# Performance work log

Hardware: AMD Instinct MI355X
Metric: run time of the kernel (lower is better)

The kernel has to match this reference:

```python
import jax, jax.numpy as jnp
import numpy as np

K = 1024          # num_embeddings
D = 128           # embedding_dim
COMMITMENT_COST = 0.25


def setup_inputs() -> dict:
    key = jax.random.key(0)
    k1, k2 = jax.random.split(key)
    inputs = jax.random.normal(k1, (16, D, 4096), dtype=jnp.float32)
    codebook = jax.random.normal(k2, (K, D), dtype=jnp.float32)
    return {"inputs": inputs, "codebook": codebook}


def reference(inputs, codebook):
    # inputs: [B, D, T]; codebook: [K, D]
    B, Dd, T = inputs.shape
    flat = jnp.transpose(inputs, (0, 2, 1)).reshape(-1, Dd)  # [N, D], N = B*T
    N = flat.shape[0]

    d = (jnp.sum(flat * flat, axis=1, keepdims=True)
         + jnp.sum(codebook * codebook, axis=1)
         - 2.0 * flat @ codebook.T)
    idx = jnp.argmin(d, axis=1)  # [N]

    # gather-based quantization (same math as one-hot @ codebook)
    quantized = codebook[idx]                                   # [N, D]
    quantized = quantized.reshape(B, T, Dd).transpose(0, 2, 1)  # [B, D, T]

    # commitment loss (quantized detached; stop_gradient irrelevant in fwd)
    e_latent_loss = jnp.mean((jax.lax.stop_gradient(quantized) - inputs) ** 2)
    loss = COMMITMENT_COST * e_latent_loss

    # straight-through estimator
    quantized_st = inputs + jax.lax.stop_gradient(quantized - inputs)

    # perplexity from code usage histogram (= mean of one-hot encodings)
    counts = jnp.zeros((codebook.shape[0],), dtype=jnp.float32).at[idx].add(1.0)
    avg_probs = counts / N
    perplexity = jnp.exp(-jnp.sum(avg_probs * jnp.log(avg_probs + 1e-10)))

    return loss, quantized_st, perplexity, idx.reshape(B, T)
```

## Files before the change

kernel.cpp:

```cpp
#include <hip/hip_runtime.h>

#define T_FULL 4096
#define D 128
#define K 1024
#define NVEC 65536
#define BDT 8388608
#define BT 128
#define NBLK (NVEC / BT)
#define KT 64
#define NIT (K / KT)
#define PLANE_B (K * D * 2)
#define TILE_B (2 * KT * D * 2)

typedef _Float16 f16x8 __attribute__((ext_vector_type(8)));
typedef float f32x4 __attribute__((ext_vector_type(4)));

#define MFMA(a, b, c) __builtin_amdgcn_mfma_f32_16x16x32_f16((a), (b), (c), 0, 0, 0)

#define GLOAD_LDS(g, l)                                                        \
  __builtin_amdgcn_global_load_lds(                                            \
      (const __attribute__((address_space(1))) unsigned int*)(g),              \
      (__attribute__((address_space(3))) unsigned int*)(l), 16, 0, 0)

__global__ __launch_bounds__(128) void prep_kernel(const float* __restrict__ cb,
    float* __restrict__ ee, _Float16* __restrict__ E1, _Float16* __restrict__ E2,
    unsigned int* __restrict__ counts, unsigned int* __restrict__ done,
    float* __restrict__ loss_acc) {
  int k = blockIdx.x, d = threadIdx.x;
  if (d == 0) {
    counts[k] = 0u;
    if (k == 0) { *done = 0u; *loss_acc = 0.f; }
  }
  float e = cb[k * D + d];
  float v = e * e;
#pragma unroll
  for (int o = 32; o > 0; o >>= 1) v += __shfl_down(v, o, 64);
  __shared__ float tmp[2];
  if ((d & 63) == 0) tmp[d >> 6] = v;
  __syncthreads();
  if (d == 0) ee[k] = tmp[0] + tmp[1];

  float s = 2.0f * e;
  _Float16 h1 = (_Float16)s;
  _Float16 h2 = (_Float16)(s - (float)h1);
  E1[k * D + d] = h1;
  E2[k * D + d] = h2;
}

__global__ __launch_bounds__(256, 2) void vq_main(
    const float* __restrict__ inp, const float* __restrict__ cb,
    const float* __restrict__ ee, const _Float16* __restrict__ Eplanes,
    unsigned int* __restrict__ counts, unsigned int* __restrict__ done,
    float* __restrict__ loss_acc, float* __restrict__ out) {
  __shared__ __align__(16) _Float16 Bs[2 * 2 * KT * D];
  __shared__ float ee_sh[K];
  __shared__ int   midx[BT];
  __shared__ float lred[4];
  __shared__ int   lastf;

  float* out_q   = out + 1;
  float* out_idx = out + 2 + BDT;

  const int tid  = threadIdx.x;
  const int lane = tid & 63;
  const int w    = tid >> 6;
  const int c    = lane & 15;
  const int q    = lane >> 4;
  const int b    = blockIdx.x >> 5;
  const int t0   = (blockIdx.x & 31) * BT;

  unsigned soff[8], slds[8];
#pragma unroll
  for (int i = 0; i < 8; ++i) {
    int flat = tid + i * 256;
    int p    = flat >> 10;
    int s    = flat & 1023;
    int code = s >> 4;
    int dgp  = s & 15;
    int dg   = dgp ^ (code & 15);
    soff[i] = (unsigned)(p * PLANE_B + code * 256 + dg * 16);
    slds[i] = (unsigned)(flat * 16);
  }
  const char* Eb = (const char*)Eplanes;

#pragma unroll
  for (int i = 0; i < 8; ++i)
    GLOAD_LDS(Eb + soff[i], (char*)Bs + slds[i]);

  f16x8 A1[2][4], A2[2][4];
  {
    const float* xin = inp + (size_t)b * D * T_FULL + t0 + w * 32 + c;
#pragma unroll
    for (int n = 0; n < 2; ++n)
#pragma unroll
      for (int dc = 0; dc < 4; ++dc) {
        f16x8 a1, a2;
#pragma unroll
        for (int j = 0; j < 8; ++j) {
          int d = dc * 32 + q * 8 + j;
          float x = xin[(size_t)d * T_FULL + n * 16];
          _Float16 h1 = (_Float16)x;
          _Float16 h2 = (_Float16)(x - (float)h1);
          a1[j] = h1; a2[j] = h2;
        }
        A1[n][dc] = a1; A2[n][dc] = a2;
      }
  }
#pragma unroll
  for (int i = tid; i < K; i += 256) ee_sh[i] = ee[i];
  __syncthreads();

  float bv[2][4];
  int   bi[2][4];
#pragma unroll
  for (int n = 0; n < 2; ++n)
#pragma unroll
    for (int r = 0; r < 4; ++r) { bv[n][r] = 3.4e38f; bi[n][r] = 0; }

  for (int it = 0; it < NIT; ++it) {
    const int kt = it * KT;
    const int bb = it & 1;

    if (it) __syncthreads();

    if (it != NIT - 1) {
      const int ktn = kt + KT;
      const unsigned lbo = (unsigned)((bb ^ 1) * TILE_B);
#pragma unroll
      for (int i = 0; i < 8; ++i)
        GLOAD_LDS(Eb + (size_t)ktn * 256 + soff[i], (char*)Bs + lbo + slds[i]);
    }

    f32x4 acc[2][4];
#pragma unroll
    for (int n = 0; n < 2; ++n)
#pragma unroll
      for (int kf = 0; kf < 4; ++kf) acc[n][kf] = (f32x4){0.f, 0.f, 0.f, 0.f};

    const char* Bp = (const char*)Bs + bb * TILE_B;
#pragma unroll
    for (int dc = 0; dc < 4; ++dc) {
      const int sw = ((dc * 4 + q) ^ c) * 16;
      f16x8 B1[4], B2[4];
#pragma unroll
      for (int kf = 0; kf < 4; ++kf) {
        const int ro = (kf * 16 + c) * 256 + sw;
        B1[kf] = *(const f16x8*)(Bp + ro);
        B2[kf] = *(const f16x8*)(Bp + 16384 + ro);
      }
#pragma unroll
      for (int n = 0; n < 2; ++n)
#pragma unroll
        for (int kf = 0; kf < 4; ++kf) {
          f32x4 a = acc[n][kf];
          a = MFMA(A1[n][dc], B1[kf], a);
          a = MFMA(A1[n][dc], B2[kf], a);
          a = MFMA(A2[n][dc], B1[kf], a);
          acc[n][kf] = a;
        }
    }

#pragma unroll
    for (int kf = 0; kf < 4; ++kf) {
      const int code = kt + kf * 16 + c;
      const float eev = ee_sh[code];
#pragma unroll
      for (int n = 0; n < 2; ++n)
#pragma unroll
        for (int r = 0; r < 4; ++r) {
          float dist = eev - acc[n][kf][r];
          if (dist < bv[n][r]) { bv[n][r] = dist; bi[n][r] = code; }
        }
    }
  }

#pragma unroll
  for (int m = 1; m <= 8; m <<= 1)
#pragma unroll
    for (int n = 0; n < 2; ++n)
#pragma unroll
      for (int r = 0; r < 4; ++r) {
        float ov = __shfl_xor(bv[n][r], m, 64);
        int   oi = __shfl_xor(bi[n][r], m, 64);
        if (ov < bv[n][r] || (ov == bv[n][r] && oi < bi[n][r])) {
          bv[n][r] = ov; bi[n][r] = oi;
        }
      }
  if (c == 0) {
#pragma unroll
    for (int n = 0; n < 2; ++n)
#pragma unroll
      for (int r = 0; r < 4; ++r)
        midx[w * 32 + n * 16 + q * 4 + r] = bi[n][r];
  }
  __syncthreads();

  if (tid < BT) {
    int ki = midx[tid];
    out_idx[(size_t)b * T_FULL + t0 + tid] = (float)ki;
    atomicAdd(&counts[ki], 1u);
  }

  float lsum = 0.f;
  {
    const int t  = tid & 127;
    const int dh = tid >> 7;
    const int kq = midx[t];
    const float* crow = cb + (size_t)kq * D + dh * 64;
    const float* xrow = inp + ((size_t)b * D + dh * 64) * T_FULL + t0 + t;
    float*       qrow = out_q + ((size_t)b * D + dh * 64) * T_FULL + t0 + t;
#pragma unroll
    for (int dd = 0; dd < 64; dd += 4) {
      float4 qv = *(const float4*)(crow + dd);
      float x0 = xrow[(size_t)(dd + 0) * T_FULL];
      float x1 = xrow[(size_t)(dd + 1) * T_FULL];
      float x2 = xrow[(size_t)(dd + 2) * T_FULL];
      float x3 = xrow[(size_t)(dd + 3) * T_FULL];
      float df;
      df = qv.x - x0; lsum = fmaf(df, df, lsum); qrow[(size_t)(dd + 0) * T_FULL] = qv.x;
      df = qv.y - x1; lsum = fmaf(df, df, lsum); qrow[(size_t)(dd + 1) * T_FULL] = qv.y;
      df = qv.z - x2; lsum = fmaf(df, df, lsum); qrow[(size_t)(dd + 2) * T_FULL] = qv.z;
      df = qv.w - x3; lsum = fmaf(df, df, lsum); qrow[(size_t)(dd + 3) * T_FULL] = qv.w;
    }
  }
#pragma unroll
  for (int o = 32; o > 0; o >>= 1) lsum += __shfl_down(lsum, o, 64);
  if (lane == 0) lred[w] = lsum;
  __syncthreads();
  if (tid == 0) {
    atomicAdd(loss_acc, lred[0] + lred[1] + lred[2] + lred[3]);
    __threadfence();
    unsigned ticket = atomicAdd(done, 1u);
    lastf = (ticket == NBLK - 1) ? 1 : 0;
  }
  __syncthreads();

  if (lastf) {
    __threadfence();
    float ent = 0.f;
#pragma unroll
    for (int i = tid; i < K; i += 256) {
      float cnt = (float)atomicAdd(&counts[i], 0u);
      float p = cnt * (1.0f / (float)NVEC);
      ent = fmaf(p, logf(p + 1e-10f), ent);
    }
#pragma unroll
    for (int o = 32; o > 0; o >>= 1) ent += __shfl_down(ent, o, 64);
    if (lane == 0) lred[w] = ent;
    __syncthreads();
    if (tid == 0) {
      float e = lred[0] + lred[1] + lred[2] + lred[3];
      float l = atomicAdd(loss_acc, 0.f);
      out[0]       = 0.25f * (l / (float)BDT);
      out[1 + BDT] = expf(-e);
    }
  }
}

extern "C" void kernel_launch(void* const* d_in, const int* in_sizes, int n_in,
                              void* d_out, int out_size, void* d_ws, size_t ws_size,
                              hipStream_t stream) {
  const float* inp = (const float*)d_in[0];
  const float* cb  = (const float*)d_in[1];
  float* out = (float*)d_out;

  char* ws = (char*)d_ws;
  unsigned int* counts  = (unsigned int*)ws;
  unsigned int* done    = (unsigned int*)(ws + 4096);
  float*        lossacc = (float*)(ws + 4160);
  float*        ee      = (float*)(ws + 8192);
  _Float16*     E1      = (_Float16*)(ws + 12288);
  _Float16*     E2      = (_Float16*)(ws + 12288 + PLANE_B);

  prep_kernel<<<K, 128, 0, stream>>>(cb, ee, E1, E2, counts, done, lossacc);
  vq_main<<<NBLK, 256, 0, stream>>>(inp, cb, ee, E1, counts, done, lossacc, out);
}
```

Baseline: 184.6 us.

## Deepen codebook LDS pipeline to four smaller buffers with manual vmcnt waits

Halves the codebook tile to 32 codes and uses four LDS buffers, prefetching two tiles ahead with explicit s_waitcnt vmcnt counts and raw s_barrier instead of __syncthreads. It also splits each accumulator into a main term and a correction term, breaking the three-MFMA dependency chain, and raises wave priority around the MFMA block. The goal is to hide global-to-LDS latency and improve MFMA issue. The risk is that the manual vmcnt counts are wrong or the barriers do not cover buffer reuse, which could cause races; smaller tiles also add per-iteration overhead.

```diff
diff --git a/kernel.cpp b/kernel.cpp
--- a/kernel.cpp
+++ b/kernel.cpp
@@ -7,10 +7,13 @@
 #define BDT 8388608
 #define BT 128
 #define NBLK (NVEC / BT)
-#define KT 64
+#define KT 32
 #define NIT (K / KT)
+#define NBUF 4
 #define PLANE_B (K * D * 2)
 #define TILE_B (2 * KT * D * 2)
+#define TPLANE (KT * D * 2)
+#define GTILE (KT * D * 2)
 
 typedef _Float16 f16x8 __attribute__((ext_vector_type(8)));
 typedef float f32x4 __attribute__((ext_vector_type(4)));
@@ -21,6 +24,9 @@
   __builtin_amdgcn_global_load_lds(                                            \
       (const __attribute__((address_space(1))) unsigned int*)(g),              \
       (__attribute__((address_space(3))) unsigned int*)(l), 16, 0, 0)
+
+#define SBAR() __builtin_amdgcn_s_barrier()
+#define SFENCE() __builtin_amdgcn_sched_barrier(0)
 
 __global__ __launch_bounds__(128) void prep_kernel(const float* __restrict__ cb,
     float* __restrict__ ee, _Float16* __restrict__ E1, _Float16* __restrict__ E2,
@@ -52,7 +58,7 @@
     const float* __restrict__ ee, const _Float16* __restrict__ Eplanes,
     unsigned int* __restrict__ counts, unsigned int* __restrict__ done,
     float* __restrict__ loss_acc, float* __restrict__ out) {
-  __shared__ __align__(16) _Float16 Bs[2 * 2 * KT * D];
+  __shared__ __align__(16) _Float16 Bs[NBUF * 2 * KT * D];
   __shared__ float ee_sh[K];
   __shared__ int   midx[BT];
   __shared__ float lred[4];
@@ -69,12 +75,12 @@
   const int b    = blockIdx.x >> 5;
   const int t0   = (blockIdx.x & 31) * BT;
 
-  unsigned soff[8], slds[8];
-#pragma unroll
-  for (int i = 0; i < 8; ++i) {
+  unsigned soff[4], slds[4];
+#pragma unroll
+  for (int i = 0; i < 4; ++i) {
     int flat = tid + i * 256;
-    int p    = flat >> 10;
-    int s    = flat & 1023;
+    int p    = flat >> 9;
+    int s    = flat & 511;
     int code = s >> 4;
     int dgp  = s & 15;
     int dg   = dgp ^ (code & 15);
@@ -84,8 +90,10 @@
   const char* Eb = (const char*)Eplanes;
 
 #pragma unroll
-  for (int i = 0; i < 8; ++i)
-    GLOAD_LDS(Eb + soff[i], (char*)Bs + slds[i]);
+  for (int t = 0; t < 2; ++t)
+#pragma unroll
+    for (int i = 0; i < 4; ++i)
+      GLOAD_LDS(Eb + (size_t)t * GTILE + soff[i], (char*)Bs + t * TILE_B + slds[i]);
 
   f16x8 A1[2][4], A2[2][4];
   {
@@ -117,62 +125,77 @@
 #pragma unroll
     for (int r = 0; r < 4; ++r) { bv[n][r] = 3.4e38f; bi[n][r] = 0; }
 
-  for (int it = 0; it < NIT; ++it) {
-    const int kt = it * KT;
-    const int bb = it & 1;
-
-    if (it) __syncthreads();
-
-    if (it != NIT - 1) {
-      const int ktn = kt + KT;
-      const unsigned lbo = (unsigned)((bb ^ 1) * TILE_B);
-#pragma unroll
-      for (int i = 0; i < 8; ++i)
-        GLOAD_LDS(Eb + (size_t)ktn * 256 + soff[i], (char*)Bs + lbo + slds[i]);
+#define COMPUTE_TILE(IT)                                                       \
+  {                                                                            \
+    const int   kt_ = (IT) * KT;                                               \
+    const char* Bp  = (const char*)Bs + ((IT) & (NBUF - 1)) * TILE_B;          \
+    f32x4 accM[2][2], accC[2][2];                                              \
+    _Pragma("unroll")                                                          \
+    for (int n = 0; n < 2; ++n)                                                \
+      _Pragma("unroll")                                                        \
+      for (int kf = 0; kf < 2; ++kf) {                                         \
+        accM[n][kf] = (f32x4){0.f, 0.f, 0.f, 0.f};                             \
+        accC[n][kf] = (f32x4){0.f, 0.f, 0.f, 0.f};                             \
+      }                                                                        \
+    __builtin_amdgcn_s_setprio(1);                                             \
+    _Pragma("unroll")                                                          \
+    for (int dc = 0; dc < 4; ++dc) {                                           \
+      const int sw = ((dc * 4 + q) ^ c) * 16;                  \
+      f16x8 B1[2], B2[2];                                                      \
+      _Pragma("unroll")                                                        \
+      for (int kf = 0; kf < 2; ++kf) {                                         \
+        const int ro = (kf * 16 + c) * 256 + sw;                               \
+        B1[kf] = *(const f16x8*)(Bp + ro);                                     \
+        B2[kf] = *(const f16x8*)(Bp + TPLANE + ro);                            \
+      }                                                                        \
+      _Pragma("unroll")                                                        \
+      for (int n = 0; n < 2; ++n)                                              \
+        _Pragma("unroll")                                                      \
+        for (int kf = 0; kf < 2; ++kf) {                                       \
+          accM[n][kf] = MFMA(A1[n][dc], B1[kf], accM[n][kf]);                  \
+          f32x4 t_ = accC[n][kf];                                              \
+          t_ = MFMA(A1[n][dc], B2[kf], t_);                                    \
+          t_ = MFMA(A2[n][dc], B1[kf], t_);                                    \
+          accC[n][kf] = t_;                                                    \
+        }                                                                      \
+    }                                                                          \
+    __builtin_amdgcn_s_setprio(0);                                             \
+    _Pragma("unroll")                                                          \
+    for (int kf = 0; kf < 2; ++kf) {                                           \
+      const int   code = kt_ + kf * 16 + c;                                    \
+      const float eev  = ee_sh[code];                                          \
+      _Pragma("unroll")                                                        \
+      for (int n = 0; n < 2; ++n)                                              \
+        _Pragma("unroll")                                                      \
+        for (int r = 0; r < 4; ++r) {                                          \
+          float dist = eev - accM[n][kf][r] - accC[n][kf][r];                  \
+          if (dist < bv[n][r]) { bv[n][r] = dist; bi[n][r] = code; }           \
+        }                                                                      \
+    }                                                                          \
+  }
+
+  for (int it = 0; it < NIT - 2; ++it) {
+    {
+      const char* gs = Eb + (size_t)(it + 2) * GTILE;
+      char*       ld = (char*)Bs + ((it + 2) & (NBUF - 1)) * TILE_B;
+#pragma unroll
+      for (int i = 0; i < 4; ++i) GLOAD_LDS(gs + soff[i], ld + slds[i]);
     }
-
-    f32x4 acc[2][4];
-#pragma unroll
-    for (int n = 0; n < 2; ++n)
-#pragma unroll
-      for (int kf = 0; kf < 4; ++kf) acc[n][kf] = (f32x4){0.f, 0.f, 0.f, 0.f};
-
-    const char* Bp = (const char*)Bs + bb * TILE_B;
-#pragma unroll
-    for (int dc = 0; dc < 4; ++dc) {
-      const int sw = ((dc * 4 + q) ^ c) * 16;
-      f16x8 B1[4], B2[4];
-#pragma unroll
-      for (int kf = 0; kf < 4; ++kf) {
-        const int ro = (kf * 16 + c) * 256 + sw;
-        B1[kf] = *(const f16x8*)(Bp + ro);
-        B2[kf] = *(const f16x8*)(Bp + 16384 + ro);
-      }
-#pragma unroll
-      for (int n = 0; n < 2; ++n)
-#pragma unroll
-        for (int kf = 0; kf < 4; ++kf) {
-          f32x4 a = acc[n][kf];
-          a = MFMA(A1[n][dc], B1[kf], a);
-          a = MFMA(A1[n][dc], B2[kf], a);
-          a = MFMA(A2[n][dc], B1[kf], a);
-          acc[n][kf] = a;
-        }
-    }
-
-#pragma unroll
-    for (int kf = 0; kf < 4; ++kf) {
-      const int code = kt + kf * 16 + c;
-      const float eev = ee_sh[code];
-#pragma unroll
-      for (int n = 0; n < 2; ++n)
-#pragma unroll
-        for (int r = 0; r < 4; ++r) {
-          float dist = eev - acc[n][kf][r];
-          if (dist < bv[n][r]) { bv[n][r] = dist; bi[n][r] = code; }
-        }
-    }
-  }
+    SFENCE();
+    asm volatile("s_waitcnt vmcnt(8)" ::: "memory");
+    SBAR();
+    SFENCE();
+    COMPUTE_TILE(it);
+  }
+  asm volatile("s_waitcnt vmcnt(4)" ::: "memory");
+  SBAR();
+  SFENCE();
+  COMPUTE_TILE(NIT - 2);
+  asm volatile("s_waitcnt vmcnt(0)" ::: "memory");
+  SBAR();
+  SFENCE();
+  COMPUTE_TILE(NIT - 1);
+#undef COMPUTE_TILE
 
 #pragma unroll
   for (int m = 1; m <= 8; m <<= 1)
```

Measured after the change: 186.2 us. Within noise of the previous version (+0.8%).

## Halve block and codebook tiles to double occupancy, split MFMA accumulator chains

Applied to the files above, without the earlier changes.

Cuts the per-block vector tile from 128 to 64 and the codebook tile from 64 to 32 codes. Each wave now handles one 16-row fragment, which shrinks the register and LDS footprint so four blocks can run per CU instead of two. The fp16 hi/lo MFMA chain is split into a main accumulator and a correction accumulator, giving two independent dependency chains for more instruction-level parallelism. In exchange, each wave reuses every LDS codebook read across fewer MFMAs, and codebook traffic from L2 doubles because twice as many blocks stream the whole codebook.

```diff
diff --git a/kernel.cpp b/kernel.cpp
--- a/kernel.cpp
+++ b/kernel.cpp
@@ -5,12 +5,14 @@
 #define K 1024
 #define NVEC 65536
 #define BDT 8388608
-#define BT 128
+#define BT 64
 #define NBLK (NVEC / BT)
-#define KT 64
+#define KT 32
 #define NIT (K / KT)
 #define PLANE_B (K * D * 2)
 #define TILE_B (2 * KT * D * 2)
+#define TPLANE (KT * D * 2)
+#define GTILE (KT * D * 2)
 
 typedef _Float16 f16x8 __attribute__((ext_vector_type(8)));
 typedef float f32x4 __attribute__((ext_vector_type(4)));
@@ -47,7 +49,7 @@
   E2[k * D + d] = h2;
 }
 
-__global__ __launch_bounds__(256, 2) void vq_main(
+__global__ __launch_bounds__(256, 4) void vq_main(
     const float* __restrict__ inp, const float* __restrict__ cb,
     const float* __restrict__ ee, const _Float16* __restrict__ Eplanes,
     unsigned int* __restrict__ counts, unsigned int* __restrict__ done,
@@ -66,15 +68,15 @@
   const int w    = tid >> 6;
   const int c    = lane & 15;
   const int q    = lane >> 4;
-  const int b    = blockIdx.x >> 5;
-  const int t0   = (blockIdx.x & 31) * BT;
-
-  unsigned soff[8], slds[8];
-#pragma unroll
-  for (int i = 0; i < 8; ++i) {
+  const int b    = blockIdx.x >> 6;
+  const int t0   = (blockIdx.x & 63) * BT;
+
+  unsigned soff[4], slds[4];
+#pragma unroll
+  for (int i = 0; i < 4; ++i) {
     int flat = tid + i * 256;
-    int p    = flat >> 10;
-    int s    = flat & 1023;
+    int p    = flat >> 9;
+    int s    = flat & 511;
     int code = s >> 4;
     int dgp  = s & 15;
     int dg   = dgp ^ (code & 15);
@@ -84,38 +86,34 @@
   const char* Eb = (const char*)Eplanes;
 
 #pragma unroll
-  for (int i = 0; i < 8; ++i)
+  for (int i = 0; i < 4; ++i)
     GLOAD_LDS(Eb + soff[i], (char*)Bs + slds[i]);
 
-  f16x8 A1[2][4], A2[2][4];
+  f16x8 A1[4], A2[4];
   {
-    const float* xin = inp + (size_t)b * D * T_FULL + t0 + w * 32 + c;
-#pragma unroll
-    for (int n = 0; n < 2; ++n)
-#pragma unroll
-      for (int dc = 0; dc < 4; ++dc) {
-        f16x8 a1, a2;
-#pragma unroll
-        for (int j = 0; j < 8; ++j) {
-          int d = dc * 32 + q * 8 + j;
-          float x = xin[(size_t)d * T_FULL + n * 16];
-          _Float16 h1 = (_Float16)x;
-          _Float16 h2 = (_Float16)(x - (float)h1);
-          a1[j] = h1; a2[j] = h2;
-        }
-        A1[n][dc] = a1; A2[n][dc] = a2;
-      }
+    const float* xin = inp + (size_t)b * D * T_FULL + t0 + w * 16 + c;
+#pragma unroll
+    for (int dc = 0; dc < 4; ++dc) {
+      f16x8 a1, a2;
+#pragma unroll
+      for (int j = 0; j < 8; ++j) {
+        int d = dc * 32 + q * 8 + j;
+        float x = xin[(size_t)d * T_FULL];
+        _Float16 h1 = (_Float16)x;
+        _Float16 h2 = (_Float16)(x - (float)h1);
+        a1[j] = h1; a2[j] = h2;
+      }
+      A1[dc] = a1; A2[dc] = a2;
+    }
   }
 #pragma unroll
   for (int i = tid; i < K; i += 256) ee_sh[i] = ee[i];
   __syncthreads();
 
-  float bv[2][4];
-  int   bi[2][4];
-#pragma unroll
-  for (int n = 0; n < 2; ++n)
-#pragma unroll
-    for (int r = 0; r < 4; ++r) { bv[n][r] = 3.4e38f; bi[n][r] = 0; }
+  float bv[4];
+  int   bi[4];
+#pragma unroll
+  for (int r = 0; r < 4; ++r) { bv[r] = 3.4e38f; bi[r] = 0; }
 
   for (int it = 0; it < NIT; ++it) {
     const int kt = it * KT;
@@ -124,74 +122,67 @@
     if (it) __syncthreads();
 
     if (it != NIT - 1) {
-      const int ktn = kt + KT;
+      const char* gs = Eb + (size_t)(it + 1) * GTILE;
       const unsigned lbo = (unsigned)((bb ^ 1) * TILE_B);
 #pragma unroll
-      for (int i = 0; i < 8; ++i)
-        GLOAD_LDS(Eb + (size_t)ktn * 256 + soff[i], (char*)Bs + lbo + slds[i]);
-    }
-
-    f32x4 acc[2][4];
-#pragma unroll
-    for (int n = 0; n < 2; ++n)
-#pragma unroll
-      for (int kf = 0; kf < 4; ++kf) acc[n][kf] = (f32x4){0.f, 0.f, 0.f, 0.f};
+      for (int i = 0; i < 4; ++i)
+        GLOAD_LDS(gs + soff[i], (char*)Bs + lbo + slds[i]);
+    }
+
+    f32x4 accM[2], accC[2];
+#pragma unroll
+    for (int kf = 0; kf < 2; ++kf) {
+      accM[kf] = (f32x4){0.f, 0.f, 0.f, 0.f};
+      accC[kf] = (f32x4){0.f, 0.f, 0.f, 0.f};
+    }
 
     const char* Bp = (const char*)Bs + bb * TILE_B;
 #pragma unroll
     for (int dc = 0; dc < 4; ++dc) {
       const int sw = ((dc * 4 + q) ^ c) * 16;
-      f16x8 B1[4], B2[4];
-#pragma unroll
-      for (int kf = 0; kf < 4; ++kf) {
+      f16x8 B1[2], B2[2];
+#pragma unroll
+      for (int kf = 0; kf < 2; ++kf) {
         const int ro = (kf * 16 + c) * 256 + sw;
         B1[kf] = *(const f16x8*)(Bp + ro);
-        B2[kf] = *(const f16x8*)(Bp + 16384 + ro);
-      }
-#pragma unroll
-      for (int n = 0; n < 2; ++n)
-#pragma unroll
-        for (int kf = 0; kf < 4; ++kf) {
-          f32x4 a = acc[n][kf];
-          a = MFMA(A1[n][dc], B1[kf], a);
-          a = MFMA(A1[n][dc], B2[kf], a);
-          a = MFMA(A2[n][dc], B1[kf], a);
-          acc[n][kf] = a;
-        }
-    }
-
-#pragma unroll
-    for (int kf = 0; kf < 4; ++kf) {
+        B2[kf] = *(const f16x8*)(Bp + TPLANE + ro);
+      }
+#pragma unroll
+      for (int kf = 0; kf < 2; ++kf) {
+        accM[kf] = MFMA(A1[dc], B1[kf], accM[kf]);
+        f32x4 t_ = accC[kf];
+        t_ = MFMA(A1[dc], B2[kf], t_);
+        t_ = MFMA(A2[dc], B1[kf], t_);
+        accC[kf] = t_;
+      }
+    }
+
+#pragma unroll
+    for (int kf = 0; kf < 2; ++kf) {
       const int code = kt + kf * 16 + c;
       const float eev = ee_sh[code];
 #pragma unroll
-      for (int n = 0; n < 2; ++n)
-#pragma unroll
-        for (int r = 0; r < 4; ++r) {
-          float dist = eev - acc[n][kf][r];
-          if (dist < bv[n][r]) { bv[n][r] = dist; bi[n][r] = code; }
-        }
+      for (int r = 0; r < 4; ++r) {
+        float dist = eev - accM[kf][r] - accC[kf][r];
+        if (dist < bv[r]) { bv[r] = dist; bi[r] = code; }
+      }
     }
   }
 
 #pragma unroll
   for (int m = 1; m <= 8; m <<= 1)
 #pragma unroll
-    for (int n = 0; n < 2; ++n)
-#pragma unroll
-      for (int r = 0; r < 4; ++r) {
-        float ov = __shfl_xor(bv[n][r], m, 64);
-        int   oi = __shfl_xor(bi[n][r], m, 64);
-        if (ov < bv[n][r] || (ov == bv[n][r] && oi < bi[n][r])) {
-          bv[n][r] = ov; bi[n][r] = oi;
-        }
-      }
+    for (int r = 0; r < 4; ++r) {
+      float ov = __shfl_xor(bv[r], m, 64);
+      int   oi = __shfl_xor(bi[r], m, 64);
+      if (ov < bv[r] || (ov == bv[r] && oi < bi[r])) {
+        bv[r] = ov; bi[r] = oi;
+      }
+    }
   if (c == 0) {
 #pragma unroll
-    for (int n = 0; n < 2; ++n)
-#pragma unroll
-      for (int r = 0; r < 4; ++r)
-        midx[w * 32 + n * 16 + q * 4 + r] = bi[n][r];
+    for (int r = 0; r < 4; ++r)
+      midx[w * 16 + q * 4 + r] = bi[r];
   }
   __syncthreads();
 
@@ -203,14 +194,14 @@
 
   float lsum = 0.f;
   {
-    const int t  = tid & 127;
-    const int dh = tid >> 7;
+    const int t  = tid & 63;
+    const int dq = tid >> 6;
     const int kq = midx[t];
-    const float* crow = cb + (size_t)kq * D + dh * 64;
-    const float* xrow = inp + ((size_t)b * D + dh * 64) * T_FULL + t0 + t;
-    float*       qrow = out_q + ((size_t)b * D + dh * 64) * T_FULL + t0 + t;
-#pragma unroll
-    for (int dd = 0; dd < 64; dd += 4) {
+    const float* crow = cb + (size_t)kq * D + dq * 32;
+    const float* xrow = inp + ((size_t)b * D + dq * 32) * T_FULL + t0 + t;
+    float*       qrow = out_q + ((size_t)b * D + dq * 32) * T_FULL + t0 + t;
+#pragma unroll
+    for (int dd = 0; dd < 32; dd += 4) {
       float4 qv = *(const float4*)(crow + dd);
       float x0 = xrow[(size_t)(dd + 0) * T_FULL];
       float x1 = xrow[(size_t)(dd + 1) * T_FULL];
```

Result: slower. 195.8 us (+6.1%).

## Split codebook search across blocks and finalize argmin in a separate kernel

Applied to the files above, without the earlier changes.

The distance/argmin kernel is split four ways over the codebook, so there are four times as many blocks, each scanning 256 codes with smaller 32-code tiles and a launch bound targeting 4 blocks per CU. Each block writes its partial best value and index to workspace, and a new finalize kernel merges the partials and does the gather, loss, histogram and perplexity. The MFMA accumulation is also split into separate main and correction accumulators. This adds more parallelism and occupancy at the cost of an extra kernel launch, workspace traffic, and recomputing the input fp16 split once per codebook slice.

```diff
diff --git a/kernel.cpp b/kernel.cpp
--- a/kernel.cpp
+++ b/kernel.cpp
@@ -6,11 +6,15 @@
 #define NVEC 65536
 #define BDT 8388608
 #define BT 128
-#define NBLK (NVEC / BT)
-#define KT 64
-#define NIT (K / KT)
+#define NTB (NVEC / BT)
+#define KSPLIT 4
+#define KR (K / KSPLIT)
+#define KT 32
+#define NIT (KR / KT)
 #define PLANE_B (K * D * 2)
 #define TILE_B (2 * KT * D * 2)
+#define TPLANE (KT * D * 2)
+#define GTILE (KT * D * 2)
 
 typedef _Float16 f16x8 __attribute__((ext_vector_type(8)));
 typedef float f32x4 __attribute__((ext_vector_type(4)));
@@ -47,44 +51,40 @@
   E2[k * D + d] = h2;
 }
 
-__global__ __launch_bounds__(256, 2) void vq_main(
-    const float* __restrict__ inp, const float* __restrict__ cb,
-    const float* __restrict__ ee, const _Float16* __restrict__ Eplanes,
-    unsigned int* __restrict__ counts, unsigned int* __restrict__ done,
-    float* __restrict__ loss_acc, float* __restrict__ out) {
+__global__ __launch_bounds__(256, 4) void vq_dist(
+    const float* __restrict__ inp, const float* __restrict__ ee,
+    const _Float16* __restrict__ Eplanes,
+    float* __restrict__ wsv, int* __restrict__ wsi) {
   __shared__ __align__(16) _Float16 Bs[2 * 2 * KT * D];
-  __shared__ float ee_sh[K];
-  __shared__ int   midx[BT];
-  __shared__ float lred[4];
-  __shared__ int   lastf;
-
-  float* out_q   = out + 1;
-  float* out_idx = out + 2 + BDT;
+  __shared__ float ee_sh[KR];
 
   const int tid  = threadIdx.x;
   const int lane = tid & 63;
   const int w    = tid >> 6;
   const int c    = lane & 15;
   const int q    = lane >> 4;
-  const int b    = blockIdx.x >> 5;
-  const int t0   = (blockIdx.x & 31) * BT;
-
-  unsigned soff[8], slds[8];
-#pragma unroll
-  for (int i = 0; i < 8; ++i) {
+  const int tb   = blockIdx.x >> 2;
+  const int ks   = blockIdx.x & 3;
+  const int b    = tb >> 5;
+  const int t0   = (tb & 31) * BT;
+  const int k0   = ks * KR;
+
+  unsigned soff[4], slds[4];
+#pragma unroll
+  for (int i = 0; i < 4; ++i) {
     int flat = tid + i * 256;
-    int p    = flat >> 10;
-    int s    = flat & 1023;
+    int p    = flat >> 9;
+    int s    = flat & 511;
     int code = s >> 4;
     int dgp  = s & 15;
     int dg   = dgp ^ (code & 15);
     soff[i] = (unsigned)(p * PLANE_B + code * 256 + dg * 16);
     slds[i] = (unsigned)(flat * 16);
   }
-  const char* Eb = (const char*)Eplanes;
-
-#pragma unroll
-  for (int i = 0; i < 8; ++i)
+  const char* Eb = (const char*)Eplanes + (size_t)k0 * 256;
+
+#pragma unroll
+  for (int i = 0; i < 4; ++i)
     GLOAD_LDS(Eb + soff[i], (char*)Bs + slds[i]);
 
   f16x8 A1[2][4], A2[2][4];
@@ -107,7 +107,7 @@
       }
   }
 #pragma unroll
-  for (int i = tid; i < K; i += 256) ee_sh[i] = ee[i];
+  for (int i = tid; i < KR; i += 256) ee_sh[i] = ee[k0 + i];
   __syncthreads();
 
   float bv[2][4];
@@ -124,51 +124,55 @@
     if (it) __syncthreads();
 
     if (it != NIT - 1) {
-      const int ktn = kt + KT;
+      const char* gs = Eb + (size_t)(it + 1) * GTILE;
       const unsigned lbo = (unsigned)((bb ^ 1) * TILE_B);
 #pragma unroll
-      for (int i = 0; i < 8; ++i)
-        GLOAD_LDS(Eb + (size_t)ktn * 256 + soff[i], (char*)Bs + lbo + slds[i]);
-    }
-
-    f32x4 acc[2][4];
+      for (int i = 0; i < 4; ++i)
+        GLOAD_LDS(gs + soff[i], (char*)Bs + lbo + slds[i]);
+    }
+
+    f32x4 accM[2][2], accC[2][2];
 #pragma unroll
     for (int n = 0; n < 2; ++n)
 #pragma unroll
-      for (int kf = 0; kf < 4; ++kf) acc[n][kf] = (f32x4){0.f, 0.f, 0.f, 0.f};
+      for (int kf = 0; kf < 2; ++kf) {
+        accM[n][kf] = (f32x4){0.f, 0.f, 0.f, 0.f};
+        accC[n][kf] = (f32x4){0.f, 0.f, 0.f, 0.f};
+      }
 
     const char* Bp = (const char*)Bs + bb * TILE_B;
 #pragma unroll
     for (int dc = 0; dc < 4; ++dc) {
       const int sw = ((dc * 4 + q) ^ c) * 16;
-      f16x8 B1[4], B2[4];
-#pragma unroll
-      for (int kf = 0; kf < 4; ++kf) {
+      f16x8 B1[2], B2[2];
+#pragma unroll
+      for (int kf = 0; kf < 2; ++kf) {
         const int ro = (kf * 16 + c) * 256 + sw;
         B1[kf] = *(const f16x8*)(Bp + ro);
-        B2[kf] = *(const f16x8*)(Bp + 16384 + ro);
+        B2[kf] = *(const f16x8*)(Bp + TPLANE + ro);
       }
 #pragma unroll
       for (int n = 0; n < 2; ++n)
 #pragma unroll
-        for (int kf = 0; kf < 4; ++kf) {
-          f32x4 a = acc[n][kf];
-          a = MFMA(A1[n][dc], B1[kf], a);
-          a = MFMA(A1[n][dc], B2[kf], a);
-          a = MFMA(A2[n][dc], B1[kf], a);
-          acc[n][kf] = a;
+        for (int kf = 0; kf < 2; ++kf) {
+          accM[n][kf] = MFMA(A1[n][dc], B1[kf], accM[n][kf]);
+          f32x4 t_ = accC[n][kf];
+          t_ = MFMA(A1[n][dc], B2[kf], t_);
+          t_ = MFMA(A2[n][dc], B1[kf], t_);
+          accC[n][kf] = t_;
         }
     }
 
 #pragma unroll
-    for (int kf = 0; kf < 4; ++kf) {
-      const int code = kt + kf * 16 + c;
-      const float eev = ee_sh[code];
+    for (int kf = 0; kf < 2; ++kf) {
+      const int lcode = kt + kf * 16 + c;
+      const int code  = k0 + lcode;
+      const float eev = ee_sh[lcode];
 #pragma unroll
       for (int n = 0; n < 2; ++n)
 #pragma unroll
         for (int r = 0; r < 4; ++r) {
-          float dist = eev - acc[n][kf][r];
+          float dist = eev - accM[n][kf][r] - accC[n][kf][r];
           if (dist < bv[n][r]) { bv[n][r] = dist; bi[n][r] = code; }
         }
     }
@@ -187,19 +191,54 @@
         }
       }
   if (c == 0) {
+    float* wv = wsv + (size_t)blockIdx.x * BT;
+    int*   wi = wsi + (size_t)blockIdx.x * BT;
 #pragma unroll
     for (int n = 0; n < 2; ++n)
 #pragma unroll
-      for (int r = 0; r < 4; ++r)
-        midx[w * 32 + n * 16 + q * 4 + r] = bi[n][r];
-  }
-  __syncthreads();
+      for (int r = 0; r < 4; ++r) {
+        const int t = w * 32 + n * 16 + q * 4 + r;
+        wv[t] = bv[n][r];
+        wi[t] = bi[n][r];
+      }
+  }
+}
+
+__global__ __launch_bounds__(256) void vq_fin(
+    const float* __restrict__ inp, const float* __restrict__ cb,
+    const float* __restrict__ wsv, const int* __restrict__ wsi,
+    unsigned int* __restrict__ counts, unsigned int* __restrict__ done,
+    float* __restrict__ loss_acc, float* __restrict__ out) {
+  __shared__ int   midx[BT];
+  __shared__ float lred[4];
+  __shared__ int   lastf;
+
+  float* out_q   = out + 1;
+  float* out_idx = out + 2 + BDT;
+
+  const int tid  = threadIdx.x;
+  const int lane = tid & 63;
+  const int w    = tid >> 6;
+  const int tb   = blockIdx.x;
+  const int b    = tb >> 5;
+  const int t0   = (tb & 31) * BT;
 
   if (tid < BT) {
-    int ki = midx[tid];
-    out_idx[(size_t)b * T_FULL + t0 + tid] = (float)ki;
-    atomicAdd(&counts[ki], 1u);
-  }
+    const float* wv = wsv + (size_t)tb * KSPLIT * BT;
+    const int*   wi = wsi + (size_t)tb * KSPLIT * BT;
+    float best = wv[tid];
+    int   bidx = wi[tid];
+#pragma unroll
+    for (int s = 1; s < KSPLIT; ++s) {
+      float v  = wv[s * BT + tid];
+      int   ii = wi[s * BT + tid];
+      if (v < best) { best = v; bidx = ii; }
+    }
+    midx[tid] = bidx;
+    out_idx[(size_t)b * T_FULL + t0 + tid] = (float)bidx;
+    atomicAdd(&counts[bidx], 1u);
+  }
+  __syncthreads();
 
   float lsum = 0.f;
   {
@@ -231,7 +270,7 @@
     atomicAdd(loss_acc, lred[0] + lred[1] + lred[2] + lred[3]);
     __threadfence();
     unsigned ticket = atomicAdd(done, 1u);
-    lastf = (ticket == NBLK - 1) ? 1 : 0;
+    lastf = (ticket == NTB - 1) ? 1 : 0;
   }
   __syncthreads();
 
@@ -271,7 +310,11 @@
   float*        ee      = (float*)(ws + 8192);
   _Float16*     E1      = (_Float16*)(ws + 12288);
   _Float16*     E2      = (_Float16*)(ws + 12288 + PLANE_B);
+  char*         pbase   = ws + 12288 + 2 * PLANE_B;
+  float*        wsv     = (float*)pbase;
+  int*          wsi     = (int*)(pbase + (size_t)NTB * KSPLIT * BT * 4);
 
   prep_kernel<<<K, 128, 0, stream>>>(cb, ee, E1, E2, counts, done, lossacc);
-  vq_main<<<NBLK, 256, 0, stream>>>(inp, cb, ee, E1, counts, done, lossacc, out);
+  vq_dist<<<NTB * KSPLIT, 256, 0, stream>>>(inp, ee, E1, wsv, wsi);
+  vq_fin<<<NTB, 256, 0, stream>>>(inp, cb, wsv, wsi, counts, done, lossacc, out);
 }
```

Result: slower. 522.4 us (+183.0%).
